# Optimization experiments

Hardware: AMD Instinct MI355X
Metric: run time of the kernel (lower is better)

## Reference

```python
import jax, jax.numpy as jnp
import numpy as np

VOXEL_LENGTH = 1.2


def grid_sample_3d_border(vol, grid):
    """torch.nn.functional.grid_sample (5D, bilinear, align_corners=False,
    padding_mode='border') with grid flattened to (B, N, 3) in (x, y, z) order.
    vol: (B, C, D, H, W). Returns (B, C, N)."""

    def sample_one(v, g):
        C, D, H, W = v.shape
        x, y, z = g[:, 0], g[:, 1], g[:, 2]
        # align_corners=False unnormalization
        ix = ((x + 1.0) * W - 1.0) * 0.5
        iy = ((y + 1.0) * H - 1.0) * 0.5
        iz = ((z + 1.0) * D - 1.0) * 0.5
        ix0f, iy0f, iz0f = jnp.floor(ix), jnp.floor(iy), jnp.floor(iz)
        wx, wy, wz = ix - ix0f, iy - iy0f, iz - iz0f
        # border padding: clamp indices, keep unclamped weights
        x0 = jnp.clip(ix0f, 0, W - 1).astype(jnp.int32)
        x1 = jnp.clip(ix0f + 1, 0, W - 1).astype(jnp.int32)
        y0 = jnp.clip(iy0f, 0, H - 1).astype(jnp.int32)
        y1 = jnp.clip(iy0f + 1, 0, H - 1).astype(jnp.int32)
        z0 = jnp.clip(iz0f, 0, D - 1).astype(jnp.int32)
        z1 = jnp.clip(iz0f + 1, 0, D - 1).astype(jnp.int32)
        vflat = v.reshape(C, D * H * W)

        def gather(zi, yi, xi):  # -> (C, N)
            return vflat[:, (zi * H + yi) * W + xi]

        out = (
            gather(z0, y0, x0) * ((1 - wz) * (1 - wy) * (1 - wx))
            + gather(z0, y0, x1) * ((1 - wz) * (1 - wy) * wx)
            + gather(z0, y1, x0) * ((1 - wz) * wy * (1 - wx))
            + gather(z0, y1, x1) * ((1 - wz) * wy * wx)
            + gather(z1, y0, x0) * (wz * (1 - wy) * (1 - wx))
            + gather(z1, y0, x1) * (wz * (1 - wy) * wx)
            + gather(z1, y1, x0) * (wz * wy * (1 - wx))
            + gather(z1, y1, x1) * (wz * wy * wx)
        )
        return out

    return jax.vmap(sample_one)(vol, grid)


def setup_inputs() -> dict:
    key = jax.random.key(0)
    ks = jax.random.split(key, 16)
    B, IMG, STEPS = 2, 64, 24
    N = IMG * IMG * STEPS
    C_IN, HID, RES = 32, 256, 32
    # points in world space, inside the voxel cube [-0.6, 0.6]
    points = jax.random.uniform(ks[0], (B, N, 3), jnp.float32) * 1.2 - 0.6
    feature_volume = jax.random.normal(ks[1], (B, C_IN, RES, RES, RES), jnp.float32)

    def lin(k, fan_in, fan_out, scale):
        kw, kb = jax.random.split(k)
        W = jax.random.uniform(kw, (fan_out, fan_in), jnp.float32, -scale, scale)
        b = jax.random.uniform(kb, (fan_out,), jnp.float32, -scale, scale)
        return W, b

    freq = 12.0
    W0, b0 = lin(ks[2], C_IN, HID, 1.0 / C_IN)  # first_layer_film_sine_init
    W1, b1 = lin(ks[3], HID, HID, float(np.sqrt(6.0 / HID) / freq))
    W2, b2 = lin(ks[4], HID, HID, float(np.sqrt(6.0 / HID) / freq))
    W3, b3 = lin(ks[5], HID, HID, float(np.sqrt(6.0 / HID) / freq))
    Wf, bf = lin(ks[6], HID, 4, float(np.sqrt(6.0 / HID) / freq))
    return {
        "points": points, "feature_volume": feature_volume,
        "W0": W0, "b0": b0, "W1": W1, "b1": b1, "W2": W2, "b2": b2,
        "W3": W3, "b3": b3, "Wf": Wf, "bf": bf,
        "img_size": 64, "num_steps": 24,
    }


def reference(points, feature_volume, W0, b0, W1, b1, W2, b2, W3, b3, Wf, bf,
              img_size, num_steps):
    grid = points / (VOXEL_LENGTH / 2.0)  # (B, N, 3) in [-1, 1]
    feats = grid_sample_3d_border(feature_volume, grid)  # (B, C, N)
    x = feats.transpose(0, 2, 1)  # (B, N, C)
    for W, b in ((W0, b0), (W1, b1), (W2, b2), (W3, b3)):
        x = jnp.sin(jnp.einsum('bnc,hc->bnh', x, W) + b)
    rgb_sigma = jnp.einsum('bnh,oh->bno', x, Wf) + bf  # (B, N, 4)
    rgb = jax.nn.sigmoid(rgb_sigma[..., :3])
    sigma = rgb_sigma[..., 3:4]
    return jnp.concatenate([rgb, sigma], axis=-1)
```

## Files before the change

kernel.cpp:

```cpp
#include <hip/hip_runtime.h>
#include <math.h>

#define THREADS 256

typedef __attribute__((ext_vector_type(4))) float f32x4;

#define INV2PI 0.15915494309189535f
#define WS     512.0f
#define INV_WS 0.001953125f

#define NCHUNK 26
#define STREAM_BYTES (NCHUNK * 8192)
#define SBIAS_BYTES 4096

__device__ __host__ __forceinline__ int sigma_k(int k) {
    return (k & 0xE1) | ((k & 0x04) << 2) | ((k & 0x18) >> 1) | (k & 0x02);
}

__device__ __forceinline__ float fast_sigmoid(float x) {
    return 1.0f / (1.0f + __expf(-x));
}

__device__ __forceinline__ float hw_sin(float x) {
    float r;
    asm("v_sin_f32 %0, %1" : "=v"(r) : "v"(x));
    return r;
}

__device__ __forceinline__ unsigned pk8_lo(float a, float b) {
    return (unsigned)__builtin_amdgcn_cvt_pk_fp8_f32(a, b, 0, false);
}
__device__ __forceinline__ unsigned pk8_hi(unsigned old, float a, float b) {
    return (unsigned)__builtin_amdgcn_cvt_pk_fp8_f32(a, b, (int)old, true);
}
__device__ __forceinline__ long long pk8x8(const float v[8]) {
    const unsigned u0 = pk8_hi(pk8_lo(v[0], v[1]), v[2], v[3]);
    const unsigned u1 = pk8_hi(pk8_lo(v[4], v[5]), v[6], v[7]);
    return (long long)(((unsigned long long)u1 << 32) | u0);
}

__global__ void build_frags(const float* __restrict__ W0,
                            const float* __restrict__ W1,
                            const float* __restrict__ W2,
                            const float* __restrict__ W3,
                            const float* __restrict__ Wf,
                            unsigned char* __restrict__ stream) {
    const int gid = blockIdx.x * 256 + threadIdx.x;
    const int f = gid >> 6;
    if (f >= 416) return;
    const int lane = gid & 63;
    const int p16 = lane & 15, g = lane >> 4;
    unsigned char* dst = stream + (size_t)f * 512 + lane * 8;

    float v[8];
    if (f < 16) {
        const float* row = W0 + (size_t)(f * 16 + p16) * 32;
#pragma unroll
        for (int i = 0; i < 8; ++i) v[i] = row[8 * g + i] * (INV2PI * WS);
    } else if (f < 400) {
        const int t = f - 16;
        const int h = t >> 7;
        const int r = t & 127;
        const int sub = r >> 4;
        const int idx = r & 15;
        const int q = sub & 1;
        const int kq = sub >> 1;
        const int ksl = idx >> 3;
        const int ntl = idx & 7;
        const int nt = q * 8 + ntl;
        const int ks = kq * 2 + ksl;
        const float* W = (h == 0) ? W1 : (h == 1) ? W2 : W3;
        const float* row = W + (size_t)(nt * 16 + p16) * 256;
#pragma unroll
        for (int i = 0; i < 8; ++i)
            v[i] = row[sigma_k(32 * ks + 8 * g + i)] * (INV2PI * WS);
    } else if (f < 408) {
        const int ks = f - 400;
        if (p16 < 4) {
            const float* row = Wf + (size_t)p16 * 256;
#pragma unroll
            for (int i = 0; i < 8; ++i) v[i] = row[sigma_k(32 * ks + 8 * g + i)] * WS;
        } else {
#pragma unroll
            for (int i = 0; i < 8; ++i) v[i] = 0.0f;
        }
    } else {
#pragma unroll
        for (int i = 0; i < 8; ++i) v[i] = 0.0f;
    }
    const long long pk = pk8x8(v);
    *(long long*)dst = pk;
}

__global__ void scale_biases(const float* __restrict__ b0, const float* __restrict__ b1,
                             const float* __restrict__ b2, const float* __restrict__ b3,
                             float* __restrict__ sb) {
    const int i = blockIdx.x * 256 + threadIdx.x;
    const int l = i >> 8, j = i & 255;
    const float* b = (l == 0) ? b0 : (l == 1) ? b1 : (l == 2) ? b2 : b3;
    sb[i] = b[j] * (INV2PI * WS);
}

__global__ void vol_chlast(const float* __restrict__ vol, float* __restrict__ dst, int nvox) {
    int v = blockIdx.x * 256 + threadIdx.x;
    if (v >= nvox) return;
    const int b = v >> 15, idx = v & 32767;
    const float* s = vol + (size_t)b * 32 * 32768 + idx;
    float* d = dst + (size_t)v * 32;
#pragma unroll
    for (int c = 0; c < 32; ++c) d[c] = s[(size_t)c * 32768];
}

#define MF8(a, b, c) __builtin_amdgcn_mfma_f32_16x16x32_fp8_fp8((a), (b), (c), 0, 0, 0)

__global__ __launch_bounds__(THREADS, 2)
void siren_pl(const float* __restrict__ points,
              const float* __restrict__ vol,
              const float* __restrict__ bfin,
              const unsigned char* __restrict__ Wstream,
              const float* __restrict__ sb,
              const float* __restrict__ volcl, int use_cl,
              float* __restrict__ out, long long total, int N) {
    __shared__ __align__(16) unsigned char ring[3 * 8192];

    const int tid = (int)threadIdx.x;
    const int w = tid >> 6;
    const int lane = tid & 63;
    const int p16 = lane & 15;
    const int g = lane >> 4;

    const long long base = (long long)blockIdx.x * 128;

    auto stage = [&](int c) {
        if (c >= NCHUNK) return;
        const unsigned char* src = Wstream + (size_t)c * 8192;
        unsigned char* dstbase = ring + (c % 3) * 8192;
#pragma unroll
        for (int q = 0; q < 2; ++q) {
            const int off = (q * 4 + w) * 1024;
            __builtin_amdgcn_global_load_lds(
                (const __attribute__((address_space(1))) unsigned int*)(src + off + lane * 16),
                (__attribute__((address_space(3))) unsigned int*)(dstbase + off),
                16, 0, 0);
        }
    };
    stage(0);
    stage(1);
    stage(2);

    long long af0[2];
    {
#pragma unroll
        for (int ptt = 0; ptt < 2; ++ptt) {
            const long long gidx = base + w * 32 + ptt * 16 + p16;
            const long long gp = gidx < total ? gidx : total - 1;
            const int bi = (int)(gp / N);
            const float* pp = points + gp * 3;
            const float sc = 1.0f / 0.6f;
            const float ix = (pp[0] * sc + 1.0f) * 16.0f - 0.5f;
            const float iy = (pp[1] * sc + 1.0f) * 16.0f - 0.5f;
            const float iz = (pp[2] * sc + 1.0f) * 16.0f - 0.5f;
            const float fx = floorf(ix), fy = floorf(iy), fz = floorf(iz);
            const float wx = ix - fx, wy = iy - fy, wz = iz - fz;
            const int x0 = (int)fminf(fmaxf(fx, 0.0f), 31.0f);
            const int x1 = (int)fminf(fmaxf(fx + 1.0f, 0.0f), 31.0f);
            const int y0 = (int)fminf(fmaxf(fy, 0.0f), 31.0f);
            const int y1 = (int)fminf(fmaxf(fy + 1.0f, 0.0f), 31.0f);
            const int z0 = (int)fminf(fmaxf(fz, 0.0f), 31.0f);
            const int z1 = (int)fminf(fmaxf(fz + 1.0f, 0.0f), 31.0f);
            const int i000 = (z0 * 32 + y0) * 32 + x0, i001 = (z0 * 32 + y0) * 32 + x1;
            const int i010 = (z0 * 32 + y1) * 32 + x0, i011 = (z0 * 32 + y1) * 32 + x1;
            const int i100 = (z1 * 32 + y0) * 32 + x0, i101 = (z1 * 32 + y0) * 32 + x1;
            const int i110 = (z1 * 32 + y1) * 32 + x0, i111 = (z1 * 32 + y1) * 32 + x1;
            const float omx = 1.0f - wx, omy = 1.0f - wy, omz = 1.0f - wz;
            const float w000 = omz * omy * omx, w001 = omz * omy * wx;
            const float w010 = omz * wy * omx,  w011 = omz * wy * wx;
            const float w100 = wz * omy * omx,  w101 = wz * omy * wx;
            const float w110 = wz * wy * omx,   w111 = wz * wy * wx;

            f32x4 a[2];
            if (use_cl) {
                const float* vb = volcl + (size_t)bi * 32768 * 32 + g * 8;
#pragma unroll
                for (int h = 0; h < 2; ++h) {
                    const float* vh = vb + h * 4;
                    a[h]  = w000 * *(const f32x4*)(vh + (size_t)i000 * 32);
                    a[h] += w001 * *(const f32x4*)(vh + (size_t)i001 * 32);
                    a[h] += w010 * *(const f32x4*)(vh + (size_t)i010 * 32);
                    a[h] += w011 * *(const f32x4*)(vh + (size_t)i011 * 32);
                    a[h] += w100 * *(const f32x4*)(vh + (size_t)i100 * 32);
                    a[h] += w101 * *(const f32x4*)(vh + (size_t)i101 * 32);
                    a[h] += w110 * *(const f32x4*)(vh + (size_t)i110 * 32);
                    a[h] += w111 * *(const f32x4*)(vh + (size_t)i111 * 32);
                }
            } else {
                const float* vb = vol + ((size_t)bi * 32 + (size_t)g * 8) * 32768;
#pragma unroll
                for (int c = 0; c < 8; ++c) {
                    const float* vc = vb + (size_t)c * 32768;
                    a[c >> 2][c & 3] =
                        vc[i000] * w000 + vc[i001] * w001 + vc[i010] * w010 + vc[i011] * w011 +
                        vc[i100] * w100 + vc[i101] * w101 + vc[i110] * w110 + vc[i111] * w111;
                }
            }
            const unsigned u0 = pk8_hi(pk8_lo(a[0][0], a[0][1]), a[0][2], a[0][3]);
            const unsigned u1 = pk8_hi(pk8_lo(a[1][0], a[1][1]), a[1][2], a[1][3]);
            af0[ptt] = (long long)(((unsigned long long)u1 << 32) | u0);
        }
    }

    f32x4 accA[2][8];
    f32x4 accB[2][8];
    long long bfr[2][8];
    long long wreg[8];

    auto frag_at = [&](int slot, int idx) -> long long {
        return *(const long long*)&ring[slot * 8192 + idx * 512 + lane * 8];
    };
    auto init_half = [&](f32x4 (&A)[2][8], const float* __restrict__ b, int ntbase) {
#pragma unroll
        for (int m = 0; m < 8; ++m) {
            const f32x4 bv = *(const f32x4*)&b[(ntbase + m) * 16 + 4 * g];
            A[0][m] = bv; A[1][m] = bv;
        }
    };
    auto pack_half = [&](f32x4 (&A)[2][8], int ksbase) {
#pragma unroll
        for (int ptt = 0; ptt < 2; ++ptt)
#pragma unroll
            for (int ks2 = 0; ks2 < 4; ++ks2) {
                const int m0 = 2 * ks2, m1 = 2 * ks2 + 1;
                float s[8];
#pragma unroll
                for (int r = 0; r < 4; ++r) {
                    s[r]     = hw_sin(A[ptt][m0][r] * INV_WS);
                    s[4 + r] = hw_sin(A[ptt][m1][r] * INV_WS);
                }
                bfr[ptt][ksbase + ks2] = pk8x8(s);
            }
    };
    auto mfma_half = [&](int kq, int ksl, f32x4 (&A)[2][8], int nslot, int nbase) {
        const long long bA = bfr[0][kq * 2 + ksl];
        const long long bB = bfr[1][kq * 2 + ksl];
        __builtin_amdgcn_s_setprio(1);
#pragma unroll
        for (int ntl = 0; ntl < 8; ++ntl) {
            A[0][ntl] = MF8(wreg[ntl], bA, A[0][ntl]);
            A[1][ntl] = MF8(wreg[ntl], bB, A[1][ntl]);
            wreg[ntl] = frag_at(nslot, nbase + ntl);
        }
        __builtin_amdgcn_s_setprio(0);
    };

    init_half(accA, sb, 0);
    init_half(accB, sb, 8);
    __syncthreads();

#pragma unroll
    for (int i = 0; i < 8; ++i) wreg[i] = frag_at(0, i);

    __builtin_amdgcn_s_setprio(1);
#pragma unroll
    for (int ntl = 0; ntl < 8; ++ntl) {
        accA[0][ntl] = MF8(wreg[ntl], af0[0], accA[0][ntl]);
        accA[1][ntl] = MF8(wreg[ntl], af0[1], accA[1][ntl]);
        wreg[ntl] = frag_at(0, 8 + ntl);
    }
#pragma unroll
    for (int ntl = 0; ntl < 8; ++ntl) {
        accB[0][ntl] = MF8(wreg[ntl], af0[0], accB[0][ntl]);
        accB[1][ntl] = MF8(wreg[ntl], af0[1], accB[1][ntl]);
        wreg[ntl] = frag_at(1, ntl);
    }
    __builtin_amdgcn_s_setprio(0);
    __syncthreads(); stage(3);

#define LCH(k, ACC, KQ)                                                \
        mfma_half(KQ, 0, ACC, ((cbase) + (k)) % 3, 8);                 \
        mfma_half(KQ, 1, ACC, ((cbase) + (k) + 1) % 3, 0);             \
        __syncthreads(); stage((cbase) + (k) + 3);

#define LAYER(CB, SBL)                                                 \
    do {                                                               \
        const int cbase = (CB);                                        \
        pack_half(accA, 0); init_half(accA, (SBL), 0);                 \
        LCH(0, accA, 0)                                                \
        pack_half(accB, 4); init_half(accB, (SBL), 8);                 \
        LCH(1, accB, 0)                                                \
        LCH(2, accA, 1)                                                \
        LCH(3, accB, 1)                                                \
        LCH(4, accA, 2)                                                \
        LCH(5, accB, 2)                                                \
        LCH(6, accA, 3)                                                \
        LCH(7, accB, 3)                                                \
    } while (0)

    LAYER(1,  sb + 256);
    LAYER(9,  sb + 512);
    LAYER(17, sb + 768);

    pack_half(accA, 0);
    pack_half(accB, 4);
    {
        f32x4 fo[2] = {{0, 0, 0, 0}, {0, 0, 0, 0}};
#pragma unroll
        for (int ks = 0; ks < 8; ++ks) {
            fo[0] = MF8(wreg[ks], bfr[0][ks], fo[0]);
            fo[1] = MF8(wreg[ks], bfr[1][ks], fo[1]);
        }
        if (g == 0) {
#pragma unroll
            for (int ptt = 0; ptt < 2; ++ptt) {
                const long long oi = base + w * 32 + ptt * 16 + p16;
                if (oi < total) {
                    float4 o;
                    o.x = fast_sigmoid(fo[ptt][0] * INV_WS + bfin[0]);
                    o.y = fast_sigmoid(fo[ptt][1] * INV_WS + bfin[1]);
                    o.z = fast_sigmoid(fo[ptt][2] * INV_WS + bfin[2]);
                    o.w = fo[ptt][3] * INV_WS + bfin[3];
                    *(float4*)(out + oi * 4) = o;
                }
            }
        }
    }
}

extern "C" void kernel_launch(void* const* d_in, const int* in_sizes, int n_in,
                              void* d_out, int out_size, void* d_ws, size_t ws_size,
                              hipStream_t stream) {
    const float* points = (const float*)d_in[0];
    const float* vol    = (const float*)d_in[1];
    const float* W0 = (const float*)d_in[2];
    const float* b0 = (const float*)d_in[3];
    const float* W1 = (const float*)d_in[4];
    const float* b1 = (const float*)d_in[5];
    const float* W2 = (const float*)d_in[6];
    const float* b2 = (const float*)d_in[7];
    const float* W3 = (const float*)d_in[8];
    const float* b3 = (const float*)d_in[9];
    const float* Wf = (const float*)d_in[10];
    const float* bf = (const float*)d_in[11];

    const int B = in_sizes[1] / (32 * 32 * 32 * 32);
    const int N = in_sizes[0] / (3 * B);
    const long long total = (long long)B * N;
    const int tiles = (int)((total + 127) / 128);

    unsigned char* Wstream = (unsigned char*)d_ws;
    float* sb = (float*)((char*)d_ws + STREAM_BYTES);
    build_frags<<<104, 256, 0, stream>>>(W0, W1, W2, W3, Wf, Wstream);
    scale_biases<<<4, 256, 0, stream>>>(b0, b1, b2, b3, sb);

    const size_t fixed = (size_t)STREAM_BYTES + SBIAS_BYTES;
    const int use_cl = (ws_size >= fixed + (size_t)B * 32768 * 32 * 4) ? 1 : 0;
    float* volcl = (float*)((char*)d_ws + fixed);
    if (use_cl) {
        const int nvox = B * 32768;
        vol_chlast<<<(nvox + 255) / 256, 256, 0, stream>>>(vol, volcl, nvox);
    }

    siren_pl<<<tiles, THREADS, 0, stream>>>(
        points, vol, bf, Wstream, sb, volcl, use_cl,
        (float*)d_out, total, N);
}
```

Baseline: 101.1 us.

## Switch hidden SIREN layers from fp8 MFMA to int8 16x16x64 MFMA

Replaces the fp8 16x16x32 MFMA path for the three hidden 256x256 layers and the final layer with int8 16x16x64 MFMA. Weights are quantized to int8 with a fixed scale, and sine activations are packed to int8 via pknorm and byte permutes. The weight stream is relaid out into 16KB chunks with a new k-permutation, and the LDS ring is doubled. Biases are now added in float after integer accumulation. The aim is to halve the number of MFMA issues per layer, at the cost of different quantization error and fixed weight scales that could saturate for some weight ranges.

```diff
diff --git a/kernel.cpp b/kernel.cpp
--- a/kernel.cpp
+++ b/kernel.cpp
@@ -4,17 +4,23 @@
 #define THREADS 256
 
 typedef __attribute__((ext_vector_type(4))) float f32x4;
+typedef __attribute__((ext_vector_type(4))) int   i32x4;
 
 #define INV2PI 0.15915494309189535f
 #define WS     512.0f
 #define INV_WS 0.001953125f
-
-#define NCHUNK 26
-#define STREAM_BYTES (NCHUNK * 8192)
+#define SW     61440.0f
+#define SWF    8192.0f
+#define QA     127.99609375f
+#define INVH   (1.0f / (SW * QA))
+#define INVF   (1.0f / (SWF * QA))
+
+#define NCHUNK 14
+#define STREAM_BYTES (NCHUNK * 16384)
 #define SBIAS_BYTES 4096
 
-__device__ __host__ __forceinline__ int sigma_k(int k) {
-    return (k & 0xE1) | ((k & 0x04) << 2) | ((k & 0x18) >> 1) | (k & 0x02);
+__device__ __host__ __forceinline__ int sigma64(int k) {
+    return (k & 0xC3) | ((k & 0x30) >> 2) | ((k & 0x0C) << 2);
 }
 
 __device__ __forceinline__ float fast_sigmoid(float x) {
@@ -33,10 +39,19 @@
 __device__ __forceinline__ unsigned pk8_hi(unsigned old, float a, float b) {
     return (unsigned)__builtin_amdgcn_cvt_pk_fp8_f32(a, b, (int)old, true);
 }
-__device__ __forceinline__ long long pk8x8(const float v[8]) {
-    const unsigned u0 = pk8_hi(pk8_lo(v[0], v[1]), v[2], v[3]);
-    const unsigned u1 = pk8_hi(pk8_lo(v[4], v[5]), v[6], v[7]);
-    return (long long)(((unsigned long long)u1 << 32) | u0);
+
+__device__ __forceinline__ unsigned pknorm(float a, float b) {
+    unsigned d;
+    asm("v_cvt_pknorm_i16_f32 %0, %1, %2" : "=v"(d) : "v"(a), "v"(b));
+    return d;
+}
+__device__ __forceinline__ int hi_bytes(unsigned lo, unsigned hi) {
+    return (int)__builtin_amdgcn_perm(hi, lo, 0x07050301u);
+}
+
+__device__ __forceinline__ signed char q8(float x) {
+    const float c = fminf(fmaxf(x, -127.0f), 127.0f);
+    return (signed char)(int)rintf(c);
 }
 
 __global__ void build_frags(const float* __restrict__ W0,
@@ -46,50 +61,69 @@
                             const float* __restrict__ Wf,
                             unsigned char* __restrict__ stream) {
     const int gid = blockIdx.x * 256 + threadIdx.x;
-    const int f = gid >> 6;
-    if (f >= 416) return;
-    const int lane = gid & 63;
-    const int p16 = lane & 15, g = lane >> 4;
-    unsigned char* dst = stream + (size_t)f * 512 + lane * 8;
-
-    float v[8];
-    if (f < 16) {
-        const float* row = W0 + (size_t)(f * 16 + p16) * 32;
-#pragma unroll
-        for (int i = 0; i < 8; ++i) v[i] = row[8 * g + i] * (INV2PI * WS);
-    } else if (f < 400) {
-        const int t = f - 16;
-        const int h = t >> 7;
-        const int r = t & 127;
-        const int sub = r >> 4;
-        const int idx = r & 15;
-        const int q = sub & 1;
-        const int kq = sub >> 1;
-        const int ksl = idx >> 3;
-        const int ntl = idx & 7;
-        const int nt = q * 8 + ntl;
-        const int ks = kq * 2 + ksl;
+    if (gid >= STREAM_BYTES / 8) return;
+    const int off = gid * 8;
+    const int c = off >> 14;
+    const int wi = off & 16383;
+    unsigned char* dst = stream + off;
+    unsigned char b[8];
+#pragma unroll
+    for (int i = 0; i < 8; ++i) b[i] = 0;
+
+    if (c == 0) {
+        if (wi < 8192) {
+            const int f = wi >> 9;
+            const int wf = wi & 511;
+            const int l = wf >> 3;
+            const int p16 = l & 15, g = l >> 4;
+            const float* row = W0 + (size_t)(f * 16 + p16) * 32;
+            float v[8];
+#pragma unroll
+            for (int i = 0; i < 8; ++i) v[i] = row[8 * g + i] * (INV2PI * WS);
+            unsigned u0 = pk8_hi(pk8_lo(v[0], v[1]), v[2], v[3]);
+            unsigned u1 = pk8_hi(pk8_lo(v[4], v[5]), v[6], v[7]);
+#pragma unroll
+            for (int i = 0; i < 4; ++i) { b[i] = (u0 >> (8 * i)) & 0xFF; b[4 + i] = (u1 >> (8 * i)) & 0xFF; }
+        }
+    } else if (c <= 12) {
+        const int t0 = c - 1;
+        const int h = t0 >> 2;
+        const int cc = t0 & 3;
+        const int tb = (cc & 1) * 8;
+        const int sbase = (cc >> 1) * 2;
+        const int fragidx = wi >> 10;
+        const int wf = wi & 1023;
+        const int l = wf >> 4;
+        const int ib = wf & 15;
+        const int ss = fragidx >> 3, tl = fragidx & 7;
+        const int n = (tb + tl) * 16 + (l & 15);
         const float* W = (h == 0) ? W1 : (h == 1) ? W2 : W3;
-        const float* row = W + (size_t)(nt * 16 + p16) * 256;
-#pragma unroll
-        for (int i = 0; i < 8; ++i)
-            v[i] = row[sigma_k(32 * ks + 8 * g + i)] * (INV2PI * WS);
-    } else if (f < 408) {
-        const int ks = f - 400;
-        if (p16 < 4) {
-            const float* row = Wf + (size_t)p16 * 256;
-#pragma unroll
-            for (int i = 0; i < 8; ++i) v[i] = row[sigma_k(32 * ks + 8 * g + i)] * WS;
-        } else {
-#pragma unroll
-            for (int i = 0; i < 8; ++i) v[i] = 0.0f;
+        const float* row = W + (size_t)n * 256;
+#pragma unroll
+        for (int i = 0; i < 8; ++i) {
+            const int k = 64 * (sbase + ss) + 16 * (l >> 4) + ib + i;
+            b[i] = (unsigned char)q8(row[sigma64(k)] * (INV2PI * SW));
         }
     } else {
-#pragma unroll
-        for (int i = 0; i < 8; ++i) v[i] = 0.0f;
+        const int fragidx = wi >> 10;
+        const int wf = wi & 1023;
+        const int l = wf >> 4;
+        const int ib = wf & 15;
+        const int r = l & 15;
+        if (fragidx < 4 && r < 4) {
+            const int s = fragidx;
+            const float* row = Wf + (size_t)r * 256;
+#pragma unroll
+            for (int i = 0; i < 8; ++i) {
+                const int k = 64 * s + 16 * (l >> 4) + ib + i;
+                b[i] = (unsigned char)q8(row[sigma64(k)] * SWF);
+            }
+        }
     }
-    const long long pk = pk8x8(v);
-    *(long long*)dst = pk;
+    unsigned long long pk = 0;
+#pragma unroll
+    for (int i = 0; i < 8; ++i) pk |= (unsigned long long)b[i] << (8 * i);
+    *(unsigned long long*)dst = pk;
 }
 
 __global__ void scale_biases(const float* __restrict__ b0, const float* __restrict__ b1,
@@ -97,8 +131,10 @@
                              float* __restrict__ sb) {
     const int i = blockIdx.x * 256 + threadIdx.x;
     const int l = i >> 8, j = i & 255;
-    const float* b = (l == 0) ? b0 : (l == 1) ? b1 : (l == 2) ? b2 : b3;
-    sb[i] = b[j] * (INV2PI * WS);
+    if (l == 0)      sb[i] = b0[j] * (INV2PI * WS);
+    else if (l == 1) sb[i] = b1[j] * INV2PI;
+    else if (l == 2) sb[i] = b2[j] * INV2PI;
+    else             sb[i] = b3[j] * INV2PI;
 }
 
 __global__ void vol_chlast(const float* __restrict__ vol, float* __restrict__ dst, int nvox) {
@@ -111,7 +147,8 @@
     for (int c = 0; c < 32; ++c) d[c] = s[(size_t)c * 32768];
 }
 
-#define MF8(a, b, c) __builtin_amdgcn_mfma_f32_16x16x32_fp8_fp8((a), (b), (c), 0, 0, 0)
+#define MF8(a, b, c)  __builtin_amdgcn_mfma_f32_16x16x32_fp8_fp8((a), (b), (c), 0, 0, 0)
+#define MFI8(a, b, c) __builtin_amdgcn_mfma_i32_16x16x64_i8((a), (b), (c), 0, 0, 0)
 
 __global__ __launch_bounds__(THREADS, 2)
 void siren_pl(const float* __restrict__ points,
@@ -121,7 +158,7 @@
               const float* __restrict__ sb,
               const float* __restrict__ volcl, int use_cl,
               float* __restrict__ out, long long total, int N) {
-    __shared__ __align__(16) unsigned char ring[3 * 8192];
+    __shared__ __align__(16) unsigned char ring[3 * 16384];
 
     const int tid = (int)threadIdx.x;
     const int w = tid >> 6;
@@ -133,10 +170,10 @@
 
     auto stage = [&](int c) {
         if (c >= NCHUNK) return;
-        const unsigned char* src = Wstream + (size_t)c * 8192;
-        unsigned char* dstbase = ring + (c % 3) * 8192;
-#pragma unroll
-        for (int q = 0; q < 2; ++q) {
+        const unsigned char* src = Wstream + (size_t)c * 16384;
+        unsigned char* dstbase = ring + (c % 3) * 16384;
+#pragma unroll
+        for (int q = 0; q < 4; ++q) {
             const int off = (q * 4 + w) * 1024;
             __builtin_amdgcn_global_load_lds(
                 (const __attribute__((address_space(1))) unsigned int*)(src + off + lane * 16),
@@ -209,104 +246,128 @@
         }
     }
 
-    f32x4 accA[2][8];
-    f32x4 accB[2][8];
-    long long bfr[2][8];
-    long long wreg[8];
-
-    auto frag_at = [&](int slot, int idx) -> long long {
-        return *(const long long*)&ring[slot * 8192 + idx * 512 + lane * 8];
-    };
-    auto init_half = [&](f32x4 (&A)[2][8], const float* __restrict__ b, int ntbase) {
+    f32x4 acc0A[2][8], acc0B[2][8];
+    i32x4 accA[2][8],  accB[2][8];
+    i32x4 S0[2], S1[2], S2[2], S3[2];
+    i32x4 wreg[8];
+
+    auto frag_i8 = [&](int slot, int idx) -> i32x4 {
+        return *(const i32x4*)&ring[slot * 16384 + idx * 1024 + lane * 16];
+    };
+    auto frag_f8 = [&](int idx) -> long long {
+        return *(const long long*)&ring[idx * 512 + lane * 8];
+    };
+    auto initf = [&](f32x4 (&A)[2][8], int ntbase) {
 #pragma unroll
         for (int m = 0; m < 8; ++m) {
-            const f32x4 bv = *(const f32x4*)&b[(ntbase + m) * 16 + 4 * g];
+            const f32x4 bv = *(const f32x4*)&sb[(ntbase + m) * 16 + 4 * g];
             A[0][m] = bv; A[1][m] = bv;
         }
     };
-    auto pack_half = [&](f32x4 (&A)[2][8], int ksbase) {
+    auto zeroacc = [&](i32x4 (&A)[2][8]) {
+        const i32x4 z = {0, 0, 0, 0};
+#pragma unroll
+        for (int m = 0; m < 8; ++m) { A[0][m] = z; A[1][m] = z; }
+    };
+    auto packL0 = [&](f32x4 (&A)[2][8], i32x4 (&Sa)[2], i32x4 (&Sb)[2]) {
 #pragma unroll
         for (int ptt = 0; ptt < 2; ++ptt)
 #pragma unroll
-            for (int ks2 = 0; ks2 < 4; ++ks2) {
-                const int m0 = 2 * ks2, m1 = 2 * ks2 + 1;
-                float s[8];
-#pragma unroll
-                for (int r = 0; r < 4; ++r) {
-                    s[r]     = hw_sin(A[ptt][m0][r] * INV_WS);
-                    s[4 + r] = hw_sin(A[ptt][m1][r] * INV_WS);
-                }
-                bfr[ptt][ksbase + ks2] = pk8x8(s);
+            for (int d = 0; d < 4; ++d) {
+                float s0 = hw_sin(A[ptt][d][0] * INV_WS);
+                float s1 = hw_sin(A[ptt][d][1] * INV_WS);
+                float s2 = hw_sin(A[ptt][d][2] * INV_WS);
+                float s3 = hw_sin(A[ptt][d][3] * INV_WS);
+                Sa[ptt][d] = hi_bytes(pknorm(s0, s1), pknorm(s2, s3));
+                s0 = hw_sin(A[ptt][4 + d][0] * INV_WS);
+                s1 = hw_sin(A[ptt][4 + d][1] * INV_WS);
+                s2 = hw_sin(A[ptt][4 + d][2] * INV_WS);
+                s3 = hw_sin(A[ptt][4 + d][3] * INV_WS);
+                Sb[ptt][d] = hi_bytes(pknorm(s0, s1), pknorm(s2, s3));
             }
     };
-    auto mfma_half = [&](int kq, int ksl, f32x4 (&A)[2][8], int nslot, int nbase) {
-        const long long bA = bfr[0][kq * 2 + ksl];
-        const long long bB = bfr[1][kq * 2 + ksl];
+    auto packH = [&](i32x4 (&A)[2][8], const float* bp, int nb,
+                     i32x4 (&Sa)[2], i32x4 (&Sb)[2]) {
+#pragma unroll
+        for (int ptt = 0; ptt < 2; ++ptt)
+#pragma unroll
+            for (int d = 0; d < 4; ++d) {
+                const f32x4 bv = *(const f32x4*)&bp[(nb + d) * 16 + 4 * g];
+                float s0 = hw_sin(fmaf((float)A[ptt][d][0], INVH, bv[0]));
+                float s1 = hw_sin(fmaf((float)A[ptt][d][1], INVH, bv[1]));
+                float s2 = hw_sin(fmaf((float)A[ptt][d][2], INVH, bv[2]));
+                float s3 = hw_sin(fmaf((float)A[ptt][d][3], INVH, bv[3]));
+                Sa[ptt][d] = hi_bytes(pknorm(s0, s1), pknorm(s2, s3));
+                const f32x4 bw = *(const f32x4*)&bp[(nb + 4 + d) * 16 + 4 * g];
+                s0 = hw_sin(fmaf((float)A[ptt][4 + d][0], INVH, bw[0]));
+                s1 = hw_sin(fmaf((float)A[ptt][4 + d][1], INVH, bw[1]));
+                s2 = hw_sin(fmaf((float)A[ptt][4 + d][2], INVH, bw[2]));
+                s3 = hw_sin(fmaf((float)A[ptt][4 + d][3], INVH, bw[3]));
+                Sb[ptt][d] = hi_bytes(pknorm(s0, s1), pknorm(s2, s3));
+            }
+    };
+    auto half_mfma = [&](const i32x4 (&S)[2], i32x4 (&A)[2][8], int nslot, int nbase) {
         __builtin_amdgcn_s_setprio(1);
 #pragma unroll
-        for (int ntl = 0; ntl < 8; ++ntl) {
-            A[0][ntl] = MF8(wreg[ntl], bA, A[0][ntl]);
-            A[1][ntl] = MF8(wreg[ntl], bB, A[1][ntl]);
-            wreg[ntl] = frag_at(nslot, nbase + ntl);
+        for (int tl = 0; tl < 8; ++tl) {
+            A[0][tl] = MFI8(wreg[tl], S[0], A[0][tl]);
+            A[1][tl] = MFI8(wreg[tl], S[1], A[1][tl]);
+            wreg[tl] = frag_i8(nslot, nbase + tl);
         }
         __builtin_amdgcn_s_setprio(0);
     };
 
-    init_half(accA, sb, 0);
-    init_half(accB, sb, 8);
+    initf(acc0A, 0);
+    initf(acc0B, 8);
     __syncthreads();
 
-#pragma unroll
-    for (int i = 0; i < 8; ++i) wreg[i] = frag_at(0, i);
-
     __builtin_amdgcn_s_setprio(1);
 #pragma unroll
     for (int ntl = 0; ntl < 8; ++ntl) {
-        accA[0][ntl] = MF8(wreg[ntl], af0[0], accA[0][ntl]);
-        accA[1][ntl] = MF8(wreg[ntl], af0[1], accA[1][ntl]);
-        wreg[ntl] = frag_at(0, 8 + ntl);
-    }
-#pragma unroll
-    for (int ntl = 0; ntl < 8; ++ntl) {
-        accB[0][ntl] = MF8(wreg[ntl], af0[0], accB[0][ntl]);
-        accB[1][ntl] = MF8(wreg[ntl], af0[1], accB[1][ntl]);
-        wreg[ntl] = frag_at(1, ntl);
+        const long long wl = frag_f8(ntl);
+        const long long wh = frag_f8(8 + ntl);
+#pragma unroll
+        for (int ptt = 0; ptt < 2; ++ptt) {
+            acc0A[ptt][ntl] = MF8(wl, af0[ptt], acc0A[ptt][ntl]);
+            acc0B[ptt][ntl] = MF8(wh, af0[ptt], acc0B[ptt][ntl]);
+        }
     }
     __builtin_amdgcn_s_setprio(0);
+#pragma unroll
+    for (int i = 0; i < 8; ++i) wreg[i] = frag_i8(1, i);
     __syncthreads(); stage(3);
 
-#define LCH(k, ACC, KQ)                                                \
-        mfma_half(KQ, 0, ACC, ((cbase) + (k)) % 3, 8);                 \
-        mfma_half(KQ, 1, ACC, ((cbase) + (k) + 1) % 3, 0);             \
-        __syncthreads(); stage((cbase) + (k) + 3);
-
-#define LAYER(CB, SBL)                                                 \
+#define PH(SA, SB, ACC, CK)                                            \
+        half_mfma(SA, ACC, (CK) % 3, 8);                               \
+        half_mfma(SB, ACC, ((CK) + 1) % 3, 0);                         \
+        __syncthreads(); stage((CK) + 3);
+
+#define LAYERX(C, PACKA, PACKB)                                        \
     do {                                                               \
-        const int cbase = (CB);                                        \
-        pack_half(accA, 0); init_half(accA, (SBL), 0);                 \
-        LCH(0, accA, 0)                                                \
-        pack_half(accB, 4); init_half(accB, (SBL), 8);                 \
-        LCH(1, accB, 0)                                                \
-        LCH(2, accA, 1)                                                \
-        LCH(3, accB, 1)                                                \
-        LCH(4, accA, 2)                                                \
-        LCH(5, accB, 2)                                                \
-        LCH(6, accA, 3)                                                \
-        LCH(7, accB, 3)                                                \
+        PACKA; zeroacc(accA);                                          \
+        PH(S0, S1, accA, (C))                                          \
+        PACKB; zeroacc(accB);                                          \
+        PH(S0, S1, accB, (C) + 1)                                      \
+        PH(S2, S3, accA, (C) + 2)                                      \
+        PH(S2, S3, accB, (C) + 3)                                      \
     } while (0)
 
-    LAYER(1,  sb + 256);
-    LAYER(9,  sb + 512);
-    LAYER(17, sb + 768);
-
-    pack_half(accA, 0);
-    pack_half(accB, 4);
+    LAYERX(1, packL0(acc0A, S0, S1), packL0(acc0B, S2, S3));
+    LAYERX(5, packH(accA, sb + 256, 0, S0, S1), packH(accB, sb + 256, 8, S2, S3));
+    LAYERX(9, packH(accA, sb + 512, 0, S0, S1), packH(accB, sb + 512, 8, S2, S3));
+
+    packH(accA, sb + 768, 0, S0, S1);
+    packH(accB, sb + 768, 8, S2, S3);
     {
-        f32x4 fo[2] = {{0, 0, 0, 0}, {0, 0, 0, 0}};
-#pragma unroll
-        for (int ks = 0; ks < 8; ++ks) {
-            fo[0] = MF8(wreg[ks], bfr[0][ks], fo[0]);
-            fo[1] = MF8(wreg[ks], bfr[1][ks], fo[1]);
+        i32x4 fo[2];
+        const i32x4 z = {0, 0, 0, 0};
+        fo[0] = z; fo[1] = z;
+#pragma unroll
+        for (int ptt = 0; ptt < 2; ++ptt) {
+            fo[ptt] = MFI8(wreg[0], S0[ptt], fo[ptt]);
+            fo[ptt] = MFI8(wreg[1], S1[ptt], fo[ptt]);
+            fo[ptt] = MFI8(wreg[2], S2[ptt], fo[ptt]);
+            fo[ptt] = MFI8(wreg[3], S3[ptt], fo[ptt]);
         }
         if (g == 0) {
 #pragma unroll
@@ -314,10 +375,10 @@
                 const long long oi = base + w * 32 + ptt * 16 + p16;
                 if (oi < total) {
                     float4 o;
-                    o.x = fast_sigmoid(fo[ptt][0] * INV_WS + bfin[0]);
-                    o.y = fast_sigmoid(fo[ptt][1] * INV_WS + bfin[1]);
-                    o.z = fast_sigmoid(fo[ptt][2] * INV_WS + bfin[2]);
-                    o.w = fo[ptt][3] * INV_WS + bfin[3];
+                    o.x = fast_sigmoid((float)fo[ptt][0] * INVF + bfin[0]);
+                    o.y = fast_sigmoid((float)fo[ptt][1] * INVF + bfin[1]);
+                    o.z = fast_sigmoid((float)fo[ptt][2] * INVF + bfin[2]);
+                    o.w = (float)fo[ptt][3] * INVF + bfin[3];
                     *(float4*)(out + oi * 4) = o;
                 }
             }
@@ -348,7 +409,8 @@
 
     unsigned char* Wstream = (unsigned char*)d_ws;
     float* sb = (float*)((char*)d_ws + STREAM_BYTES);
-    build_frags<<<104, 256, 0, stream>>>(W0, W1, W2, W3, Wf, Wstream);
+    build_frags<<<(STREAM_BYTES / 8 + 255) / 256, 256, 0, stream>>>(
+        W0, W1, W2, W3, Wf, Wstream);
     scale_biases<<<4, 256, 0, stream>>>(b0, b1, b2, b3, sb);
 
     const size_t fixed = (size_t)STREAM_BYTES + SBIAS_BYTES;
```

Result: faster. 90.74 us, median of 3 (-10.2%).
